# Kernel tuning notes

Measured on AMD Instinct MI355X. Metric: run time of the kernel, lower is better.

The kernel has to match this reference:

```python
import jax, jax.numpy as jnp
import numpy as np

REG = 0.01
LN2 = 0.6931471805599453  # ln(2), for log2(sigmoid(x)) = log_sigmoid(x)/ln(2)


def setup_inputs() -> dict:
    key = jax.random.key(0)
    k1, k2, k3, k4, k5 = jax.random.split(key, 5)
    NUM_USER, NUM_ITEM, F, B = 1000000, 1000000, 64, 16384
    init_mean, init_stdev = 0.0, 0.01
    embed_user = init_mean + init_stdev * jax.random.normal(k1, (NUM_USER, F), dtype=jnp.float32)
    embed_item = init_mean + init_stdev * jax.random.normal(k2, (NUM_ITEM, F), dtype=jnp.float32)
    u = jax.random.randint(k3, (B,), 0, NUM_USER, dtype=jnp.int32)
    i = jax.random.randint(k4, (B,), 0, NUM_ITEM, dtype=jnp.int32)
    j = jax.random.randint(k5, (B,), 0, NUM_ITEM, dtype=jnp.int32)
    return {"embed_user": embed_user, "embed_item": embed_item, "u": u, "i": i, "j": j}


def reference(embed_user, embed_item, u, i, j):
    U = embed_user[u]          # [B, F] gathered user rows
    I = embed_item[i]          # [B, F] positive item rows
    J = embed_item[j]          # [B, F] negative item rows
    # torch.mm(U, I.t()).sum(dim=-1): row-sum of the BxB score matrix,
    # computed without materializing the BxB intermediate.
    y_ui = jnp.einsum('bf,cf->b', U, I)   # [B]
    y_uj = jnp.einsum('bf,cf->b', U, J)   # [B]
    regularizer = REG * (jnp.sum(U ** 2) + jnp.sum(I ** 2) + jnp.sum(J ** 2))
    # log2(sigmoid(x)) done stably as log_sigmoid(x) / ln(2)
    loss = regularizer - jnp.sum(jax.nn.log_sigmoid(y_ui - y_uj)) / LN2
    return (y_ui, y_uj, loss)
```

## Files before the change

### kernel.cpp

```cpp
#include <hip/hip_runtime.h>
#include <hip/hip_cooperative_groups.h>
#include <math.h>

namespace cg = cooperative_groups;

#define F 64
#define REG_C 0.01f
#define INV_LN2 1.4426950408889634f


template<int RPB>
__global__ __launch_bounds__(256, 1) void k_fused(
    const float* __restrict__ embed_user,
    const float* __restrict__ embed_item,
    const int* __restrict__ uu,
    const int* __restrict__ ii,
    const int* __restrict__ jj,
    float* __restrict__ wsA,
    float* __restrict__ wsB,
    float* __restrict__ wsC,
    float* __restrict__ out,
    int Bn)
{
    cg::grid_group grid = cg::this_grid();
    const int G    = gridDim.x;
    const int t    = threadIdx.x;
    const int q    = t & 15;
    const int rg   = t >> 4;
    const int wave = t >> 6, lane = t & 63;
    const int base = blockIdx.x * RPB;

    __shared__ int idxI[RPB], idxJ[RPB], idxU[RPB];
    if (t < RPB)          idxI[t] = (base + t < Bn) ? ii[base + t] : -1;
    else if (t < 2 * RPB) { const int r = t - RPB;     idxJ[r] = (base + r < Bn) ? jj[base + r] : -1; }
    else if (t < 3 * RPB) { const int r = t - 2 * RPB; idxU[r] = (base + r < Bn) ? uu[base + r] : -1; }
    __syncthreads();

    float4 Ur[RPB / 16];
    #pragma unroll
    for (int k = 0; k < RPB / 16; ++k) {
        const int bu = idxU[rg + k * 16];
        Ur[k] = (bu >= 0) ? ((const float4*)(embed_user + (size_t)bu * F))[q]
                          : make_float4(0.f, 0.f, 0.f, 0.f);
    }

    float4 aI = make_float4(0.f, 0.f, 0.f, 0.f);
    float4 aJ = make_float4(0.f, 0.f, 0.f, 0.f);
    float sqI = 0.f, sqJ = 0.f;
    #pragma unroll
    for (int k = 0; k < RPB / 16; ++k) {
        const int r  = rg + k * 16;
        const int bi = idxI[r];
        const int bj = idxJ[r];
        if (bi >= 0) {
            const float4 vi = ((const float4*)(embed_item + (size_t)bi * F))[q];
            aI.x += vi.x; aI.y += vi.y; aI.z += vi.z; aI.w += vi.w;
            sqI += vi.x*vi.x + vi.y*vi.y + vi.z*vi.z + vi.w*vi.w;
        }
        if (bj >= 0) {
            const float4 vj = ((const float4*)(embed_item + (size_t)bj * F))[q];
            aJ.x += vj.x; aJ.y += vj.y; aJ.z += vj.z; aJ.w += vj.w;
            sqJ += vj.x*vj.x + vj.y*vj.y + vj.z*vj.z + vj.w*vj.w;
        }
    }

    __shared__ float sI[F], sJ[F];
    if (t < F) { sI[t] = 0.f; sJ[t] = 0.f; }
    __syncthreads();
    atomicAdd(&sI[q*4+0], aI.x);
    atomicAdd(&sI[q*4+1], aI.y);
    atomicAdd(&sI[q*4+2], aI.z);
    atomicAdd(&sI[q*4+3], aI.w);
    atomicAdd(&sJ[q*4+0], aJ.x);
    atomicAdd(&sJ[q*4+1], aJ.y);
    atomicAdd(&sJ[q*4+2], aJ.z);
    atomicAdd(&sJ[q*4+3], aJ.w);

    for (int o = 32; o > 0; o >>= 1) {
        sqI += __shfl_down(sqI, o);
        sqJ += __shfl_down(sqJ, o);
    }
    __shared__ float wI[4], wJ[4];
    if (lane == 0) { wI[wave] = sqI; wJ[wave] = sqJ; }
    __syncthreads();

    if (t < 2 * F)
        wsA[(size_t)t * G + blockIdx.x] = (t < F) ? sI[t] : sJ[t - F];
    if (t == 0) {
        wsB[blockIdx.x]     = wI[0] + wI[1] + wI[2] + wI[3];
        wsB[G + blockIdx.x] = wJ[0] + wJ[1] + wJ[2] + wJ[3];
    }

    __threadfence();
    grid.sync();

    __shared__ float sIJ[2 * F];
    if (t < 2 * F) {
        const float* row = wsA + (size_t)t * G;
        float4 a4 = make_float4(0.f, 0.f, 0.f, 0.f);
        int p = 0;
        for (; p + 4 <= G; p += 4) {
            const float4 v = *(const float4*)(row + p);
            a4.x += v.x; a4.y += v.y; a4.z += v.z; a4.w += v.w;
        }
        float a = a4.x + a4.y + a4.z + a4.w;
        for (; p < G; ++p) a += row[p];
        sIJ[t] = a;
    }
    __syncthreads();

    const float4 sIq = ((const float4*)sIJ)[q];
    const float4 sJq = ((const float4*)(sIJ + F))[q];

    float accLog = 0.f, accU2 = 0.f;
    #pragma unroll
    for (int k = 0; k < RPB / 16; ++k) {
        const int r  = rg + k * 16;
        const int bu = idxU[r];
        if (bu >= 0) {
            const float4 Uq = Ur[k];
            float pi = Uq.x*sIq.x + Uq.y*sIq.y + Uq.z*sIq.z + Uq.w*sIq.w;
            float pj = Uq.x*sJq.x + Uq.y*sJq.y + Uq.z*sJq.z + Uq.w*sJq.w;
            float u2 = Uq.x*Uq.x + Uq.y*Uq.y + Uq.z*Uq.z + Uq.w*Uq.w;
            for (int o = 1; o < 16; o <<= 1) {
                pi += __shfl_xor(pi, o);
                pj += __shfl_xor(pj, o);
                u2 += __shfl_xor(u2, o);
            }
            if (q == 0) {
                const int b = base + r;
                out[b]      = pi;
                out[Bn + b] = pj;
                const float x  = pi - pj;
                const float ls = fminf(x, 0.f) - log1pf(__expf(-fabsf(x)));
                accLog += ls;
                accU2  += u2;
            }
        }
    }
    for (int o = 32; o > 0; o >>= 1) {
        accLog += __shfl_down(accLog, o);
        accU2  += __shfl_down(accU2, o);
    }
    __shared__ float wL[4], wU[4];
    if (lane == 0) { wL[wave] = accLog; wU[wave] = accU2; }
    __syncthreads();
    if (t == 0) {
        wsC[blockIdx.x]     = wU[0] + wU[1] + wU[2] + wU[3];
        wsC[G + blockIdx.x] = wL[0] + wL[1] + wL[2] + wL[3];
    }

    __threadfence();
    grid.sync();

    if (blockIdx.x == 0) {
        float sq = 0.f, u2 = 0.f, lg = 0.f;
        for (int p = t; p < 2 * G; p += 256) sq += wsB[p];
        for (int p = t; p < G; p += 256) { u2 += wsC[p]; lg += wsC[G + p]; }
        for (int o = 32; o > 0; o >>= 1) {
            sq += __shfl_down(sq, o);
            u2 += __shfl_down(u2, o);
            lg += __shfl_down(lg, o);
        }
        __shared__ float fS[4], fU[4], fL[4];
        if (lane == 0) { fS[wave] = sq; fU[wave] = u2; fL[wave] = lg; }
        __syncthreads();
        if (t == 0) {
            const float reg = REG_C * (fS[0]+fS[1]+fS[2]+fS[3] + fU[0]+fU[1]+fU[2]+fU[3]);
            out[2 * Bn] = reg - (fL[0]+fL[1]+fL[2]+fL[3]) * INV_LN2;
        }
    }
}


template<int RPB>
__global__ __launch_bounds__(256) void k_sum_items(
    const float* __restrict__ embed_item,
    const int* __restrict__ ii, const int* __restrict__ jj,
    float* __restrict__ wsA, float* __restrict__ wsB, int Bn, int G1)
{
    const int t = threadIdx.x, q = t & 15, rg = t >> 4;
    const int base = blockIdx.x * RPB;
    __shared__ int idx[2 * RPB];
    if (t < RPB)          idx[t] = (base + t < Bn) ? ii[base + t] : -1;
    else if (t < 2 * RPB) idx[t] = (base + (t - RPB) < Bn) ? jj[base + (t - RPB)] : -1;
    __syncthreads();
    float4 aI = make_float4(0,0,0,0), aJ = make_float4(0,0,0,0);
    float sqI = 0.f, sqJ = 0.f;
    #pragma unroll
    for (int k = 0; k < RPB / 16; ++k) {
        const int r = rg + k * 16;
        const int bi = idx[r], bj = idx[RPB + r];
        if (bi >= 0) {
            const float4 vi = ((const float4*)(embed_item + (size_t)bi * F))[q];
            aI.x += vi.x; aI.y += vi.y; aI.z += vi.z; aI.w += vi.w;
            sqI += vi.x*vi.x + vi.y*vi.y + vi.z*vi.z + vi.w*vi.w;
        }
        if (bj >= 0) {
            const float4 vj = ((const float4*)(embed_item + (size_t)bj * F))[q];
            aJ.x += vj.x; aJ.y += vj.y; aJ.z += vj.z; aJ.w += vj.w;
            sqJ += vj.x*vj.x + vj.y*vj.y + vj.z*vj.z + vj.w*vj.w;
        }
    }
    __shared__ float sI[F], sJ[F];
    if (t < F) { sI[t] = 0.f; sJ[t] = 0.f; }
    __syncthreads();
    atomicAdd(&sI[q*4+0], aI.x); atomicAdd(&sI[q*4+1], aI.y);
    atomicAdd(&sI[q*4+2], aI.z); atomicAdd(&sI[q*4+3], aI.w);
    atomicAdd(&sJ[q*4+0], aJ.x); atomicAdd(&sJ[q*4+1], aJ.y);
    atomicAdd(&sJ[q*4+2], aJ.z); atomicAdd(&sJ[q*4+3], aJ.w);
    for (int o = 32; o > 0; o >>= 1) { sqI += __shfl_down(sqI, o); sqJ += __shfl_down(sqJ, o); }
    __shared__ float wI[4], wJ[4];
    const int wave = t >> 6, lane = t & 63;
    if (lane == 0) { wI[wave] = sqI; wJ[wave] = sqJ; }
    __syncthreads();
    if (t < 2 * F) wsA[(size_t)t * G1 + blockIdx.x] = (t < F) ? sI[t] : sJ[t - F];
    if (t == 0) {
        wsB[blockIdx.x]      = wI[0]+wI[1]+wI[2]+wI[3];
        wsB[G1 + blockIdx.x] = wJ[0]+wJ[1]+wJ[2]+wJ[3];
    }
}

template<int RPB>
__global__ __launch_bounds__(256) void k_dots(
    const float* __restrict__ embed_user, const int* __restrict__ uu,
    const float* __restrict__ wsA, float* __restrict__ wsC,
    float* __restrict__ out, int Bn, int G1)
{
    const int t = threadIdx.x;
    const int base = blockIdx.x * RPB;
    __shared__ float sIJ[2 * F];
    __shared__ int idx[RPB];
    if (t < RPB) idx[t] = (base + t < Bn) ? uu[base + t] : -1;
    if (t < 2 * F) {
        const float* row = wsA + (size_t)t * G1;
        float4 a4 = make_float4(0,0,0,0);
        int p = 0;
        for (; p + 4 <= G1; p += 4) {
            const float4 v = *(const float4*)(row + p);
            a4.x += v.x; a4.y += v.y; a4.z += v.z; a4.w += v.w;
        }
        float a = a4.x + a4.y + a4.z + a4.w;
        for (; p < G1; ++p) a += row[p];
        sIJ[t] = a;
    }
    __syncthreads();
    const int q = t & 15, rg = t >> 4;
    const float4 sIq = ((const float4*)sIJ)[q];
    const float4 sJq = ((const float4*)(sIJ + F))[q];
    float accLog = 0.f, accU2 = 0.f;
    #pragma unroll
    for (int k = 0; k < RPB / 16; ++k) {
        const int r = rg + k * 16;
        const int bu = idx[r];
        if (bu >= 0) {
            const float4 Uq = ((const float4*)(embed_user + (size_t)bu * F))[q];
            float pi = Uq.x*sIq.x + Uq.y*sIq.y + Uq.z*sIq.z + Uq.w*sIq.w;
            float pj = Uq.x*sJq.x + Uq.y*sJq.y + Uq.z*sJq.z + Uq.w*sJq.w;
            float u2 = Uq.x*Uq.x + Uq.y*Uq.y + Uq.z*Uq.z + Uq.w*Uq.w;
            for (int o = 1; o < 16; o <<= 1) {
                pi += __shfl_xor(pi, o); pj += __shfl_xor(pj, o); u2 += __shfl_xor(u2, o);
            }
            if (q == 0) {
                const int b = base + r;
                out[b] = pi; out[Bn + b] = pj;
                const float x = pi - pj;
                accLog += fminf(x, 0.f) - log1pf(__expf(-fabsf(x)));
                accU2  += u2;
            }
        }
    }
    for (int o = 32; o > 0; o >>= 1) { accLog += __shfl_down(accLog, o); accU2 += __shfl_down(accU2, o); }
    __shared__ float wL[4], wU[4];
    const int wave = t >> 6, lane = t & 63;
    if (lane == 0) { wL[wave] = accLog; wU[wave] = accU2; }
    __syncthreads();
    if (t == 0) {
        const int G2 = gridDim.x;
        wsC[blockIdx.x]      = wU[0]+wU[1]+wU[2]+wU[3];
        wsC[G2 + blockIdx.x] = wL[0]+wL[1]+wL[2]+wL[3];
    }
}

__global__ __launch_bounds__(256) void k_finalize(
    const float* __restrict__ wsB, const float* __restrict__ wsC,
    float* __restrict__ out, int Bn, int G1, int G2)
{
    const int t = threadIdx.x;
    float sq = 0.f, u2 = 0.f, lg = 0.f;
    for (int p = t; p < 2 * G1; p += 256) sq += wsB[p];
    for (int p = t; p < G2; p += 256) { u2 += wsC[p]; lg += wsC[G2 + p]; }
    for (int o = 32; o > 0; o >>= 1) {
        sq += __shfl_down(sq, o); u2 += __shfl_down(u2, o); lg += __shfl_down(lg, o);
    }
    __shared__ float wS[4], wU[4], wL[4];
    const int wave = t >> 6, lane = t & 63;
    if (lane == 0) { wS[wave] = sq; wU[wave] = u2; wL[wave] = lg; }
    __syncthreads();
    if (t == 0) {
        const float reg = REG_C * (wS[0]+wS[1]+wS[2]+wS[3] + wU[0]+wU[1]+wU[2]+wU[3]);
        out[2 * Bn] = reg - (wL[0]+wL[1]+wL[2]+wL[3]) * INV_LN2;
    }
}

extern "C" void kernel_launch(void* const* d_in, const int* in_sizes, int n_in,
                              void* d_out, int out_size, void* d_ws, size_t ws_size,
                              hipStream_t stream) {
    const float* eu = (const float*)d_in[0];
    const float* ei = (const float*)d_in[1];
    const int*   u  = (const int*)d_in[2];
    const int*   ii = (const int*)d_in[3];
    const int*   jj = (const int*)d_in[4];
    float* out = (float*)d_out;
    float* ws  = (float*)d_ws;
    const int Bn = in_sizes[2];

    constexpr int RPB = 64;
    const int G = (Bn + RPB - 1) / RPB;
    float* wsA = ws;
    float* wsB = wsA + (size_t)2 * F * G;
    float* wsC = wsB + (size_t)2 * G;

    if (G <= 1024) {
        void* args[] = { (void*)&eu, (void*)&ei, (void*)&u, (void*)&ii, (void*)&jj,
                         (void*)&wsA, (void*)&wsB, (void*)&wsC, (void*)&out, (void*)&Bn };
        hipError_t e = hipLaunchCooperativeKernel(
            reinterpret_cast<const void*>(&k_fused<RPB>),
            dim3(G), dim3(256), args, 0, stream);
        if (e == hipSuccess) return;
    }
    k_sum_items<RPB><<<G, 256, 0, stream>>>(ei, ii, jj, wsA, wsB, Bn, G);
    k_dots<RPB><<<G, 256, 0, stream>>>(eu, u, wsA, wsC, out, Bn, G);
    k_finalize<<<1, 256, 0, stream>>>(wsB, wsC, out, Bn, G, G);
}
```

Baseline: 507.4 us.

## Replace cooperative grid-sync kernel with two kernels and last-block finalize

Drops the cooperative launch with two grid.sync barriers. The work is now split into an item-sum kernel and a dot-product kernel, and the final reduction is done by whichever block finishes last, detected with an atomic counter. Item gathers are issued up front into registers so the loads overlap. The intent is to remove the grid-wide barrier cost and the cooperative launch overhead, and to allow more than one block per CU by dropping launch_bounds min-blocks=1. In exchange it adds an extra kernel launch, and the user-row loads no longer overlap with the item phase.

```diff
diff --git a/kernel.cpp b/kernel.cpp
--- a/kernel.cpp
+++ b/kernel.cpp
@@ -1,8 +1,5 @@
 #include <hip/hip_runtime.h>
-#include <hip/hip_cooperative_groups.h>
 #include <math.h>
-
-namespace cg = cooperative_groups;
 
 #define F 64
 #define REG_C 0.01f
@@ -10,37 +7,37 @@
 
 
 template<int RPB>
-__global__ __launch_bounds__(256, 1) void k_fused(
-    const float* __restrict__ embed_user,
+__global__ __launch_bounds__(256) void k_sum_items(
     const float* __restrict__ embed_item,
-    const int* __restrict__ uu,
     const int* __restrict__ ii,
     const int* __restrict__ jj,
     float* __restrict__ wsA,
     float* __restrict__ wsB,
-    float* __restrict__ wsC,
-    float* __restrict__ out,
-    int Bn)
+    int* __restrict__ cnt,
+    int Bn, int G)
 {
-    cg::grid_group grid = cg::this_grid();
-    const int G    = gridDim.x;
-    const int t    = threadIdx.x;
-    const int q    = t & 15;
-    const int rg   = t >> 4;
-    const int wave = t >> 6, lane = t & 63;
+    const int t  = threadIdx.x;
+    const int q  = t & 15;
+    const int rg = t >> 4;
     const int base = blockIdx.x * RPB;
-
-    __shared__ int idxI[RPB], idxJ[RPB], idxU[RPB];
-    if (t < RPB)          idxI[t] = (base + t < Bn) ? ii[base + t] : -1;
-    else if (t < 2 * RPB) { const int r = t - RPB;     idxJ[r] = (base + r < Bn) ? jj[base + r] : -1; }
-    else if (t < 3 * RPB) { const int r = t - 2 * RPB; idxU[r] = (base + r < Bn) ? uu[base + r] : -1; }
-    __syncthreads();
-
-    float4 Ur[RPB / 16];
-    #pragma unroll
-    for (int k = 0; k < RPB / 16; ++k) {
-        const int bu = idxU[rg + k * 16];
-        Ur[k] = (bu >= 0) ? ((const float4*)(embed_user + (size_t)bu * F))[q]
+    constexpr int K = RPB / 16;
+
+    if (blockIdx.x == 0 && t == 0) *cnt = 0;
+
+    __shared__ int idx[2 * RPB];
+    if (t < RPB)          idx[t] = (base + t < Bn) ? ii[base + t] : -1;
+    else if (t < 2 * RPB) idx[t] = (base + (t - RPB) < Bn) ? jj[base + (t - RPB)] : -1;
+    __syncthreads();
+
+    float4 vI[K], vJ[K];
+    #pragma unroll
+    for (int k = 0; k < K; ++k) {
+        const int r  = rg + k * 16;
+        const int bi = idx[r];
+        const int bj = idx[RPB + r];
+        vI[k] = (bi >= 0) ? ((const float4*)(embed_item + (size_t)bi * F))[q]
+                          : make_float4(0.f, 0.f, 0.f, 0.f);
+        vJ[k] = (bj >= 0) ? ((const float4*)(embed_item + (size_t)bj * F))[q]
                           : make_float4(0.f, 0.f, 0.f, 0.f);
     }
 
@@ -48,20 +45,11 @@
     float4 aJ = make_float4(0.f, 0.f, 0.f, 0.f);
     float sqI = 0.f, sqJ = 0.f;
     #pragma unroll
-    for (int k = 0; k < RPB / 16; ++k) {
-        const int r  = rg + k * 16;
-        const int bi = idxI[r];
-        const int bj = idxJ[r];
-        if (bi >= 0) {
-            const float4 vi = ((const float4*)(embed_item + (size_t)bi * F))[q];
-            aI.x += vi.x; aI.y += vi.y; aI.z += vi.z; aI.w += vi.w;
-            sqI += vi.x*vi.x + vi.y*vi.y + vi.z*vi.z + vi.w*vi.w;
-        }
-        if (bj >= 0) {
-            const float4 vj = ((const float4*)(embed_item + (size_t)bj * F))[q];
-            aJ.x += vj.x; aJ.y += vj.y; aJ.z += vj.z; aJ.w += vj.w;
-            sqJ += vj.x*vj.x + vj.y*vj.y + vj.z*vj.z + vj.w*vj.w;
-        }
+    for (int k = 0; k < K; ++k) {
+        aI.x += vI[k].x; aI.y += vI[k].y; aI.z += vI[k].z; aI.w += vI[k].w;
+        sqI += vI[k].x*vI[k].x + vI[k].y*vI[k].y + vI[k].z*vI[k].z + vI[k].w*vI[k].w;
+        aJ.x += vJ[k].x; aJ.y += vJ[k].y; aJ.z += vJ[k].z; aJ.w += vJ[k].w;
+        sqJ += vJ[k].x*vJ[k].x + vJ[k].y*vJ[k].y + vJ[k].z*vJ[k].z + vJ[k].w*vJ[k].w;
     }
 
     __shared__ float sI[F], sJ[F];
@@ -81,6 +69,7 @@
         sqJ += __shfl_down(sqJ, o);
     }
     __shared__ float wI[4], wJ[4];
+    const int wave = t >> 6, lane = t & 63;
     if (lane == 0) { wI[wave] = sqI; wJ[wave] = sqJ; }
     __syncthreads();
 
@@ -90,9 +79,37 @@
         wsB[blockIdx.x]     = wI[0] + wI[1] + wI[2] + wI[3];
         wsB[G + blockIdx.x] = wJ[0] + wJ[1] + wJ[2] + wJ[3];
     }
-
-    __threadfence();
-    grid.sync();
+}
+
+template<int RPB>
+__global__ __launch_bounds__(256) void k_dots_fin(
+    const float* __restrict__ embed_user,
+    const int* __restrict__ uu,
+    const float* __restrict__ wsA,
+    const float* __restrict__ wsB,
+    float* __restrict__ wsC,
+    int* __restrict__ cnt,
+    float* __restrict__ out,
+    int Bn, int G)
+{
+    const int t  = threadIdx.x;
+    const int q  = t & 15;
+    const int rg = t >> 4;
+    const int wave = t >> 6, lane = t & 63;
+    const int base = blockIdx.x * RPB;
+    constexpr int K = RPB / 16;
+
+    __shared__ int idxU[RPB];
+    if (t < RPB) idxU[t] = (base + t < Bn) ? uu[base + t] : -1;
+    __syncthreads();
+
+    float4 Ur[K];
+    #pragma unroll
+    for (int k = 0; k < K; ++k) {
+        const int bu = idxU[rg + k * 16];
+        Ur[k] = (bu >= 0) ? ((const float4*)(embed_user + (size_t)bu * F))[q]
+                          : make_float4(0.f, 0.f, 0.f, 0.f);
+    }
 
     __shared__ float sIJ[2 * F];
     if (t < 2 * F) {
@@ -114,10 +131,9 @@
 
     float accLog = 0.f, accU2 = 0.f;
     #pragma unroll
-    for (int k = 0; k < RPB / 16; ++k) {
-        const int r  = rg + k * 16;
-        const int bu = idxU[r];
-        if (bu >= 0) {
+    for (int k = 0; k < K; ++k) {
+        const int r = rg + k * 16;
+        if (idxU[r] >= 0) {
             const float4 Uq = Ur[k];
             float pi = Uq.x*sIq.x + Uq.y*sIq.y + Uq.z*sIq.z + Uq.w*sIq.w;
             float pj = Uq.x*sJq.x + Uq.y*sJq.y + Uq.z*sJq.z + Uq.w*sJq.w;
@@ -131,9 +147,8 @@
                 const int b = base + r;
                 out[b]      = pi;
                 out[Bn + b] = pj;
-                const float x  = pi - pj;
-                const float ls = fminf(x, 0.f) - log1pf(__expf(-fabsf(x)));
-                accLog += ls;
+                const float x = pi - pj;
+                accLog += fminf(x, 0.f) - log1pf(__expf(-fabsf(x)));
                 accU2  += u2;
             }
         }
@@ -145,15 +160,19 @@
     __shared__ float wL[4], wU[4];
     if (lane == 0) { wL[wave] = accLog; wU[wave] = accU2; }
     __syncthreads();
+
+    __shared__ int isLast;
     if (t == 0) {
         wsC[blockIdx.x]     = wU[0] + wU[1] + wU[2] + wU[3];
         wsC[G + blockIdx.x] = wL[0] + wL[1] + wL[2] + wL[3];
-    }
-
-    __threadfence();
-    grid.sync();
-
-    if (blockIdx.x == 0) {
+        __threadfence();
+        const int prev = atomicAdd(cnt, 1);
+        isLast = ((prev % G) == G - 1);
+    }
+    __syncthreads();
+
+    if (isLast) {
+        __threadfence();
         float sq = 0.f, u2 = 0.f, lg = 0.f;
         for (int p = t; p < 2 * G; p += 256) sq += wsB[p];
         for (int p = t; p < G; p += 256) { u2 += wsC[p]; lg += wsC[G + p]; }
@@ -166,140 +185,10 @@
         if (lane == 0) { fS[wave] = sq; fU[wave] = u2; fL[wave] = lg; }
         __syncthreads();
         if (t == 0) {
-            const float reg = REG_C * (fS[0]+fS[1]+fS[2]+fS[3] + fU[0]+fU[1]+fU[2]+fU[3]);
+            const float reg = REG_C * (fS[0]+fS[1]+fS[2]+fS[3] +
+                                       fU[0]+fU[1]+fU[2]+fU[3]);
             out[2 * Bn] = reg - (fL[0]+fL[1]+fL[2]+fL[3]) * INV_LN2;
         }
-    }
-}
-
-
-template<int RPB>
-__global__ __launch_bounds__(256) void k_sum_items(
-    const float* __restrict__ embed_item,
-    const int* __restrict__ ii, const int* __restrict__ jj,
-    float* __restrict__ wsA, float* __restrict__ wsB, int Bn, int G1)
-{
-    const int t = threadIdx.x, q = t & 15, rg = t >> 4;
-    const int base = blockIdx.x * RPB;
-    __shared__ int idx[2 * RPB];
-    if (t < RPB)          idx[t] = (base + t < Bn) ? ii[base + t] : -1;
-    else if (t < 2 * RPB) idx[t] = (base + (t - RPB) < Bn) ? jj[base + (t - RPB)] : -1;
-    __syncthreads();
-    float4 aI = make_float4(0,0,0,0), aJ = make_float4(0,0,0,0);
-    float sqI = 0.f, sqJ = 0.f;
-    #pragma unroll
-    for (int k = 0; k < RPB / 16; ++k) {
-        const int r = rg + k * 16;
-        const int bi = idx[r], bj = idx[RPB + r];
-        if (bi >= 0) {
-            const float4 vi = ((const float4*)(embed_item + (size_t)bi * F))[q];
-            aI.x += vi.x; aI.y += vi.y; aI.z += vi.z; aI.w += vi.w;
-            sqI += vi.x*vi.x + vi.y*vi.y + vi.z*vi.z + vi.w*vi.w;
-        }
-        if (bj >= 0) {
-            const float4 vj = ((const float4*)(embed_item + (size_t)bj * F))[q];
-            aJ.x += vj.x; aJ.y += vj.y; aJ.z += vj.z; aJ.w += vj.w;
-            sqJ += vj.x*vj.x + vj.y*vj.y + vj.z*vj.z + vj.w*vj.w;
-        }
-    }
-    __shared__ float sI[F], sJ[F];
-    if (t < F) { sI[t] = 0.f; sJ[t] = 0.f; }
-    __syncthreads();
-    atomicAdd(&sI[q*4+0], aI.x); atomicAdd(&sI[q*4+1], aI.y);
-    atomicAdd(&sI[q*4+2], aI.z); atomicAdd(&sI[q*4+3], aI.w);
-    atomicAdd(&sJ[q*4+0], aJ.x); atomicAdd(&sJ[q*4+1], aJ.y);
-    atomicAdd(&sJ[q*4+2], aJ.z); atomicAdd(&sJ[q*4+3], aJ.w);
-    for (int o = 32; o > 0; o >>= 1) { sqI += __shfl_down(sqI, o); sqJ += __shfl_down(sqJ, o); }
-    __shared__ float wI[4], wJ[4];
-    const int wave = t >> 6, lane = t & 63;
-    if (lane == 0) { wI[wave] = sqI; wJ[wave] = sqJ; }
-    __syncthreads();
-    if (t < 2 * F) wsA[(size_t)t * G1 + blockIdx.x] = (t < F) ? sI[t] : sJ[t - F];
-    if (t == 0) {
-        wsB[blockIdx.x]      = wI[0]+wI[1]+wI[2]+wI[3];
-        wsB[G1 + blockIdx.x] = wJ[0]+wJ[1]+wJ[2]+wJ[3];
-    }
-}
-
-template<int RPB>
-__global__ __launch_bounds__(256) void k_dots(
-    const float* __restrict__ embed_user, const int* __restrict__ uu,
-    const float* __restrict__ wsA, float* __restrict__ wsC,
-    float* __restrict__ out, int Bn, int G1)
-{
-    const int t = threadIdx.x;
-    const int base = blockIdx.x * RPB;
-    __shared__ float sIJ[2 * F];
-    __shared__ int idx[RPB];
-    if (t < RPB) idx[t] = (base + t < Bn) ? uu[base + t] : -1;
-    if (t < 2 * F) {
-        const float* row = wsA + (size_t)t * G1;
-        float4 a4 = make_float4(0,0,0,0);
-        int p = 0;
-        for (; p + 4 <= G1; p += 4) {
-            const float4 v = *(const float4*)(row + p);
-            a4.x += v.x; a4.y += v.y; a4.z += v.z; a4.w += v.w;
-        }
-        float a = a4.x + a4.y + a4.z + a4.w;
-        for (; p < G1; ++p) a += row[p];
-        sIJ[t] = a;
-    }
-    __syncthreads();
-    const int q = t & 15, rg = t >> 4;
-    const float4 sIq = ((const float4*)sIJ)[q];
-    const float4 sJq = ((const float4*)(sIJ + F))[q];
-    float accLog = 0.f, accU2 = 0.f;
-    #pragma unroll
-    for (int k = 0; k < RPB / 16; ++k) {
-        const int r = rg + k * 16;
-        const int bu = idx[r];
-        if (bu >= 0) {
-            const float4 Uq = ((const float4*)(embed_user + (size_t)bu * F))[q];
-            float pi = Uq.x*sIq.x + Uq.y*sIq.y + Uq.z*sIq.z + Uq.w*sIq.w;
-            float pj = Uq.x*sJq.x + Uq.y*sJq.y + Uq.z*sJq.z + Uq.w*sJq.w;
-            float u2 = Uq.x*Uq.x + Uq.y*Uq.y + Uq.z*Uq.z + Uq.w*Uq.w;
-            for (int o = 1; o < 16; o <<= 1) {
-                pi += __shfl_xor(pi, o); pj += __shfl_xor(pj, o); u2 += __shfl_xor(u2, o);
-            }
-            if (q == 0) {
-                const int b = base + r;
-                out[b] = pi; out[Bn + b] = pj;
-                const float x = pi - pj;
-                accLog += fminf(x, 0.f) - log1pf(__expf(-fabsf(x)));
-                accU2  += u2;
-            }
-        }
-    }
-    for (int o = 32; o > 0; o >>= 1) { accLog += __shfl_down(accLog, o); accU2 += __shfl_down(accU2, o); }
-    __shared__ float wL[4], wU[4];
-    const int wave = t >> 6, lane = t & 63;
-    if (lane == 0) { wL[wave] = accLog; wU[wave] = accU2; }
-    __syncthreads();
-    if (t == 0) {
-        const int G2 = gridDim.x;
-        wsC[blockIdx.x]      = wU[0]+wU[1]+wU[2]+wU[3];
-        wsC[G2 + blockIdx.x] = wL[0]+wL[1]+wL[2]+wL[3];
-    }
-}
-
-__global__ __launch_bounds__(256) void k_finalize(
-    const float* __restrict__ wsB, const float* __restrict__ wsC,
-    float* __restrict__ out, int Bn, int G1, int G2)
-{
-    const int t = threadIdx.x;
-    float sq = 0.f, u2 = 0.f, lg = 0.f;
-    for (int p = t; p < 2 * G1; p += 256) sq += wsB[p];
-    for (int p = t; p < G2; p += 256) { u2 += wsC[p]; lg += wsC[G2 + p]; }
-    for (int o = 32; o > 0; o >>= 1) {
-        sq += __shfl_down(sq, o); u2 += __shfl_down(u2, o); lg += __shfl_down(lg, o);
-    }
-    __shared__ float wS[4], wU[4], wL[4];
-    const int wave = t >> 6, lane = t & 63;
-    if (lane == 0) { wS[wave] = sq; wU[wave] = u2; wL[wave] = lg; }
-    __syncthreads();
-    if (t == 0) {
-        const float reg = REG_C * (wS[0]+wS[1]+wS[2]+wS[3] + wU[0]+wU[1]+wU[2]+wU[3]);
-        out[2 * Bn] = reg - (wL[0]+wL[1]+wL[2]+wL[3]) * INV_LN2;
     }
 }
 
@@ -317,19 +206,12 @@
 
     constexpr int RPB = 64;
     const int G = (Bn + RPB - 1) / RPB;
+
     float* wsA = ws;
     float* wsB = wsA + (size_t)2 * F * G;
     float* wsC = wsB + (size_t)2 * G;
-
-    if (G <= 1024) {
-        void* args[] = { (void*)&eu, (void*)&ei, (void*)&u, (void*)&ii, (void*)&jj,
-                         (void*)&wsA, (void*)&wsB, (void*)&wsC, (void*)&out, (void*)&Bn };
-        hipError_t e = hipLaunchCooperativeKernel(
-            reinterpret_cast<const void*>(&k_fused<RPB>),
-            dim3(G), dim3(256), args, 0, stream);
-        if (e == hipSuccess) return;
-    }
-    k_sum_items<RPB><<<G, 256, 0, stream>>>(ei, ii, jj, wsA, wsB, Bn, G);
-    k_dots<RPB><<<G, 256, 0, stream>>>(eu, u, wsA, wsC, out, Bn, G);
-    k_finalize<<<1, 256, 0, stream>>>(wsB, wsC, out, Bn, G, G);
+    int*   cnt = (int*)(wsC + (size_t)2 * G);
+
+    k_sum_items<RPB><<<G, 256, 0, stream>>>(ei, ii, jj, wsA, wsB, cnt, Bn, G);
+    k_dots_fin<RPB><<<G, 256, 0, stream>>>(eu, u, wsA, wsB, wsC, cnt, out, Bn, G);
 }
```

Result: faster. 406.6 us (-19.9%).
